# Optimization experiments

Measured on AMD Instinct MI355X. Metric: run time of the kernel, lower is better.

The kernel has to match this reference:

```python
import jax, jax.numpy as jnp
import numpy as np

B, S, D, H, L = 2, 4096, 768, 12, 4
DFF, WIN, MAXPOS = 3072, 256, 4098
DH = D // H
W1 = WIN // 2            # one-sided window = 128
NC = S // W1             # number of query chunks = 32
EPS = 1e-12              # LongformerConfig default layer_norm_eps
SCALE = 1.0 / float(np.sqrt(DH))


def _ln(x, g, b):
    m = x.mean(-1, keepdims=True)
    v = ((x - m) ** 2).mean(-1, keepdims=True)
    return (x - m) / jnp.sqrt(v + EPS) * g + b


def _fwd(inputs, lengths, pos_emb, tok_emb, ln_emb_g, ln_emb_b,
         Wq, bq, Wk, bk, Wv, bv, Wo, bo, ln1_g, ln1_b,
         Wi, bi, Wf, bf, ln2_g, ln2_b):
    # embeddings: roberta-style position ids start at padding_idx+1 = 2
    x = inputs + pos_emb[2:2 + S][None] + tok_emb[0][None, None]
    x = _ln(x, ln_emb_g, ln_emb_b)

    mask = jnp.arange(S)[None, :] < lengths[:, None]            # [B,S] valid tokens
    idx = jnp.arange(NC)[:, None] * W1 + jnp.arange(3 * W1)     # [NC,3W] into padded keys
    jglob = idx - W1                                            # global key positions
    key_valid = (jglob >= 0)[None] & (jglob[None] < lengths[:, None, None])  # [B,NC,3W]
    qpos = jnp.arange(W1)[:, None]
    kpos = jnp.arange(3 * W1)[None, :]
    band = (kpos >= qpos) & (kpos <= qpos + 2 * W1)             # [W,3W] sliding band
    valid = band[None, None, None] & key_valid[:, None, :, None, :]  # [B,1,NC,W,3W]
    qmask = mask.reshape(B, NC, W1).astype(inputs.dtype)

    for l in range(L):
        q = (x @ Wq[l] + bq[l]).reshape(B, S, H, DH) * SCALE
        k = (x @ Wk[l] + bk[l]).reshape(B, S, H, DH)
        v = (x @ Wv[l] + bv[l]).reshape(B, S, H, DH)
        kp = jnp.pad(k, ((0, 0), (W1, W1), (0, 0), (0, 0)))
        vp = jnp.pad(v, ((0, 0), (W1, W1), (0, 0), (0, 0)))
        kc = jnp.take(kp, idx, axis=1)                          # [B,NC,3W,H,DH]
        vc = jnp.take(vp, idx, axis=1)
        qc = q.reshape(B, NC, W1, H, DH)
        scores = jnp.einsum('bcqhd,bckhd->bhcqk', qc, kc)       # [B,H,NC,W,3W]
        scores = jnp.where(valid, scores, -1e9)
        probs = jax.nn.softmax(scores, axis=-1)
        probs = probs * qmask[:, None, :, :, None]              # zero padded query rows (HF behavior)
        ctx = jnp.einsum('bhcqk,bckhd->bcqhd', probs, vc).reshape(B, S, D)
        x = _ln(x + ctx @ Wo[l] + bo[l], ln1_g[l], ln1_b[l])
        h = jax.nn.gelu(x @ Wi[l] + bi[l], approximate=False)
        x = _ln(x + h @ Wf[l] + bf[l], ln2_g[l], ln2_b[l])
    return x


def setup_inputs() -> dict:
    ks = jax.random.split(jax.random.key(0), 16)
    s = jnp.float32(0.02)
    f = jax.random.normal
    return {
        'inputs': f(ks[0], (B, S, D), jnp.float32),
        'lengths': jax.random.randint(ks[1], (B,), S // 2, S + 1),
        'pos_emb': s * f(ks[2], (MAXPOS, D), jnp.float32),
        'tok_emb': s * f(ks[3], (1, D), jnp.float32),
        'ln_emb_g': jnp.ones((D,), jnp.float32), 'ln_emb_b': jnp.zeros((D,), jnp.float32),
        'Wq': s * f(ks[4], (L, D, D), jnp.float32), 'bq': jnp.zeros((L, D), jnp.float32),
        'Wk': s * f(ks[5], (L, D, D), jnp.float32), 'bk': jnp.zeros((L, D), jnp.float32),
        'Wv': s * f(ks[6], (L, D, D), jnp.float32), 'bv': jnp.zeros((L, D), jnp.float32),
        'Wo': s * f(ks[7], (L, D, D), jnp.float32), 'bo': jnp.zeros((L, D), jnp.float32),
        'ln1_g': jnp.ones((L, D), jnp.float32), 'ln1_b': jnp.zeros((L, D), jnp.float32),
        'Wi': s * f(ks[8], (L, D, DFF), jnp.float32), 'bi': jnp.zeros((L, DFF), jnp.float32),
        'Wf': s * f(ks[9], (L, DFF, D), jnp.float32), 'bf': jnp.zeros((L, D), jnp.float32),
        'ln2_g': jnp.ones((L, D), jnp.float32), 'ln2_b': jnp.zeros((L, D), jnp.float32),
    }


def reference(inputs, lengths, pos_emb, tok_emb, ln_emb_g, ln_emb_b,
              Wq, bq, Wk, bk, Wv, bv, Wo, bo, ln1_g, ln1_b,
              Wi, bi, Wf, bf, ln2_g, ln2_b):
    return _fwd(inputs, lengths, pos_emb, tok_emb, ln_emb_g, ln_emb_b,
                Wq, bq, Wk, bk, Wv, bv, Wo, bo, ln1_g, ln1_b,
                Wi, bi, Wf, bf, ln2_g, ln2_b)
```

## Files before the change

### kernel.cpp

```cpp
#include <hip/hip_runtime.h>
#include <cstdint>

#define S_LEN 4096
#define D_MODEL 768
#define NHEAD 12
#define DHE 64
#define DFF_ 3072
#define NL 4
#define W1_ 128
#define NC_ 32
#define QKVN 2304

typedef __attribute__((ext_vector_type(8))) short v8s;
typedef __attribute__((ext_vector_type(4))) short v4s;
typedef __attribute__((ext_vector_type(4))) float v4f;

__device__ __forceinline__ short f2bf(float f) {
  union { float f; unsigned u; } x; x.f = f;
  unsigned r = x.u + 0x7fffu + ((x.u >> 16) & 1u);
  return (short)(r >> 16);
}

__device__ __forceinline__ float b2f(short s) {
  union { unsigned u; float f; } x; x.u = ((unsigned)(unsigned short)s) << 16;
  return x.f;
}

__device__ __forceinline__ void load_lds16(const short* g, short* l) {
  __builtin_amdgcn_global_load_lds((const __attribute__((address_space(1))) void*)g,
                                   (__attribute__((address_space(3))) void*)l, 16, 0, 0);
}

template<int NB, int EPI, int WRV>
__global__ __launch_bounds__(512, 4)
void gemm128(const short* __restrict__ A, const short* __restrict__ Bt,
             const float* __restrict__ bias, void* __restrict__ outp,
             short* __restrict__ vtw, int M, int N, int K)
{
  constexpr int CF = NB / 64;
  constexpr int BI = NB / 64;
  constexpr int SI = 2 + BI;
  constexpr int ABUF = 128 * 64;
  constexpr int BBUF = NB * 64;
  __shared__ short sA[2 * ABUF];
  __shared__ short sB[2 * BBUF];
  const int tid = threadIdx.x;
  const int lane = tid & 63, wid = tid >> 6;
  const int g = lane >> 4, l16 = lane & 15;
  const int wr = wid >> 2, wc = wid & 3;
  const int nt = K >> 6;

  const int gx = gridDim.x;
  const int nwg = gx * gridDim.y;
  const int p = blockIdx.y * gx + blockIdx.x;
  const int q8 = nwg >> 3;
  const int lb = (p & 7) * q8 + (p >> 3);
  const int bn_ = lb % gx, bm_ = lb / gx;

  const short* Ab = A + (size_t)(bm_ * 128) * K;
  const short* Bb = Bt + (size_t)(bn_ * NB) * K;

  const short* gAp[2];
  short* lAp[2];
  const short* gBp[BI];
  short* lBp[BI];
#pragma unroll
  for (int i = 0; i < 2; ++i) {
    const int byte = i * 8192 + tid * 16;
    const int row = byte >> 7;
    const int lir = (byte & 127) ^ ((row & 7) << 4);
    gAp[i] = Ab + (size_t)row * K + (lir >> 1);
    lAp[i] = &sA[(i * 8192 + wid * 1024) >> 1];
  }
#pragma unroll
  for (int i = 0; i < BI; ++i) {
    const int byte = i * 8192 + tid * 16;
    const int row = byte >> 7;
    const int lir = (byte & 127) ^ ((row & 7) << 4);
    gBp[i] = Bb + (size_t)row * K + (lir >> 1);
    lBp[i] = &sB[(i * 8192 + wid * 1024) >> 1];
  }
  auto stage = [&](int bufi) {
#pragma unroll
    for (int i = 0; i < 2; ++i) {
      load_lds16(gAp[i], lAp[i] + bufi * ABUF);
      gAp[i] += 64;
    }
#pragma unroll
    for (int i = 0; i < BI; ++i) {
      load_lds16(gBp[i], lBp[i] + bufi * BBUF);
      gBp[i] += 64;
    }
  };

  const int swz = (l16 & 7) << 4;
  const char* aB[2];
  const char* bB[2];
#pragma unroll
  for (int kk = 0; kk < 2; ++kk) {
    const int koff = ((g * 16) ^ swz) ^ (kk * 64);
    aB[kk] = (const char*)sA + (wr * 64 + l16) * 128 + koff;
    bB[kk] = (const char*)sB + (wc * (CF * 16) + l16) * 128 + koff;
  }

  v4f acc[4][CF] = {};

  stage(0);
  stage(1);
  asm volatile("s_waitcnt vmcnt(%0)" :: "i"(SI) : "memory");
  __builtin_amdgcn_s_barrier();

#define GITER(CUR, T)                                                          \
  {                                                                            \
    v8s fa[2][4], fb[2][CF];                                                   \
    _Pragma("unroll")                                                          \
    for (int kk = 0; kk < 2; ++kk) {                                           \
      _Pragma("unroll")                                                        \
      for (int m = 0; m < 4; ++m)                                              \
        fa[kk][m] = *(const v8s*)(aB[kk] + (CUR) * (2 * ABUF) + m * 2048);     \
      _Pragma("unroll")                                                        \
      for (int n = 0; n < CF; ++n)                                             \
        fb[kk][n] = *(const v8s*)(bB[kk] + (CUR) * (2 * BBUF) + n * 2048);     \
    }                                                                          \
    asm volatile("s_waitcnt lgkmcnt(0)" ::: "memory");                         \
    __builtin_amdgcn_sched_barrier(0);                                         \
    __builtin_amdgcn_s_barrier();                                              \
    if ((T) + 2 < nt) stage(CUR);                                              \
    __builtin_amdgcn_sched_barrier(0);                                         \
    __builtin_amdgcn_s_setprio(1);                                             \
    _Pragma("unroll")                                                          \
    for (int kk = 0; kk < 2; ++kk)                                             \
      _Pragma("unroll")                                                        \
      for (int m = 0; m < 4; ++m)                                              \
        _Pragma("unroll")                                                      \
        for (int n = 0; n < CF; ++n)                                           \
          acc[m][n] = __builtin_amdgcn_mfma_f32_16x16x32_bf16(fa[kk][m], fb[kk][n], acc[m][n], 0, 0, 0); \
    __builtin_amdgcn_s_setprio(0);                                             \
    __builtin_amdgcn_sched_barrier(0);                                         \
    if ((T) + 2 < nt) {                                                        \
      asm volatile("s_waitcnt vmcnt(%0)" :: "i"(SI) : "memory");               \
    } else if ((T) + 1 < nt) {                                                 \
      asm volatile("s_waitcnt vmcnt(0)" ::: "memory");                         \
    }                                                                          \
    if ((T) + 1 < nt) __builtin_amdgcn_s_barrier();                            \
  }

  for (int t = 0; t < nt; t += 2) {
    GITER(0, t);
    GITER(1, t + 1);
  }
#undef GITER

  const int row0 = bm_ * 128 + wr * 64;
  const int col0 = bn_ * NB + wc * (CF * 16);
#pragma unroll
  for (int m = 0; m < 4; ++m)
#pragma unroll
    for (int n = 0; n < CF; ++n) {
      const int col = col0 + n * 16 + l16;
      const float bc = bias[col];
      short pk4[4];
#pragma unroll
      for (int r = 0; r < 4; ++r) {
        const int row = row0 + m * 16 + g * 4 + r;
        const float v = acc[m][n][r] + bc;
        short o;
        if (EPI == 2) {
          const float e = __expf(1.5957691216057308f * (v + 0.044715f * v * v * v));
          o = f2bf(v - v / (1.0f + e));
        } else {
          o = f2bf(v);
        }
        ((short*)outp)[(size_t)row * N + col] = o;
        pk4[r] = o;
      }
      if (WRV) {
        if (col0 >= 1536) {
          const int cc = col - 1536;
          const int h = cc >> 6, d = cc & 63;
          const int rowm = row0 + m * 16 + g * 4;
          const int b = rowm >> 12, s = rowm & (S_LEN - 1);
          v4s pk = { pk4[0], pk4[1], pk4[2], pk4[3] };
          *(v4s*)&vtw[(((size_t)b * NHEAD + h) * DHE + d) * S_LEN + s] = pk;
        }
      }
    }
}

__global__ __launch_bounds__(256)
void qkvo_trans(const float* __restrict__ Wq, const float* __restrict__ Wk,
                const float* __restrict__ Wv, const float* __restrict__ Wo,
                short* __restrict__ wqkvt, short* __restrict__ wot)
{
  __shared__ float t[32][33];
  const int n0 = blockIdx.x * 32, k0 = blockIdx.y * 32;
  const int l = blockIdx.z & 3, m = blockIdx.z >> 2;
  const size_t DD = (size_t)D_MODEL * D_MODEL;
  const size_t QL = (size_t)QKVN * D_MODEL;
  const float* src = (m == 0 ? Wq : m == 1 ? Wk : m == 2 ? Wv : Wo) + (size_t)l * DD;
  short* dst = (m < 3) ? (wqkvt + (size_t)l * QL + (size_t)m * D_MODEL * D_MODEL)
                       : (wot + (size_t)l * DD);
  const float scale = (m == 0) ? 0.125f : 1.0f;
  const int tx = threadIdx.x, ty = threadIdx.y;
#pragma unroll
  for (int i = 0; i < 4; ++i)
    t[ty + 8*i][tx] = src[(size_t)(k0 + ty + 8*i) * D_MODEL + n0 + tx];
  __syncthreads();
#pragma unroll
  for (int i = 0; i < 4; ++i)
    dst[(size_t)(n0 + ty + 8*i) * D_MODEL + k0 + tx] = f2bf(t[tx][ty + 8*i] * scale);
}

__global__ __launch_bounds__(256)
void transpose_w(const float* __restrict__ in, short* __restrict__ out, int K, int N,
                 size_t in_ls, size_t out_ls, float scale)
{
  __shared__ float t[32][33];
  const int n0 = blockIdx.x * 32, k0 = blockIdx.y * 32;
  const float* src = in + (size_t)blockIdx.z * in_ls;
  short* dst = out + (size_t)blockIdx.z * out_ls;
  const int tx = threadIdx.x, ty = threadIdx.y;
#pragma unroll
  for (int i = 0; i < 4; ++i)
    t[ty + 8*i][tx] = src[(size_t)(k0 + ty + 8*i) * N + n0 + tx];
  __syncthreads();
#pragma unroll
  for (int i = 0; i < 4; ++i)
    dst[(size_t)(n0 + ty + 8*i) * K + k0 + tx] = f2bf(t[tx][ty + 8*i] * scale);
}

__global__ void prep_bias(const float* __restrict__ bq, const float* __restrict__ bk,
                          const float* __restrict__ bv, float* __restrict__ out)
{
  const int l = blockIdx.x, p = blockIdx.y, c = threadIdx.x;
  const float* s = p == 0 ? bq : (p == 1 ? bk : bv);
  out[(l * 3 + p) * 768 + c] = s[l * 768 + c] * (p == 0 ? 0.125f : 1.0f);
}

template<int MODE, int FINAL>
__global__ __launch_bounds__(256)
void ln_kernel(const void* __restrict__ in0, const void* __restrict__ in1,
               const float* __restrict__ in2,
               const float* __restrict__ gamma, const float* __restrict__ beta,
               float* __restrict__ outf, short* __restrict__ outb)
{
  __shared__ float red[8];
  const int row = blockIdx.x;
  const int tid = threadIdx.x;
  const int wave = tid >> 6, lane = tid & 63;
  float v[3];
#pragma unroll
  for (int i = 0; i < 3; ++i) {
    const int c = tid + i * 256;
    const size_t idx = (size_t)row * D_MODEL + c;
    if (MODE == 0) {
      const int s = row & (S_LEN - 1);
      v[i] = ((const float*)in0)[idx] + ((const float*)in1)[(size_t)(2 + s) * D_MODEL + c] + in2[c];
    } else {
      v[i] = b2f(((const short*)in0)[idx]) + b2f(((const short*)in1)[idx]);
    }
  }
  float sum = v[0] + v[1] + v[2];
#pragma unroll
  for (int m = 1; m < 64; m <<= 1) sum += __shfl_xor(sum, m, 64);
  if (lane == 0) red[wave] = sum;
  __syncthreads();
  const float mean = (red[0] + red[1] + red[2] + red[3]) * (1.0f / 768.0f);
  float sq = 0.f;
#pragma unroll
  for (int i = 0; i < 3; ++i) { float d = v[i] - mean; sq += d * d; }
#pragma unroll
  for (int m = 1; m < 64; m <<= 1) sq += __shfl_xor(sq, m, 64);
  if (lane == 0) red[4 + wave] = sq;
  __syncthreads();
  const float var = (red[4] + red[5] + red[6] + red[7]) * (1.0f / 768.0f);
  const float rstd = 1.0f / sqrtf(var + 1e-12f);
#pragma unroll
  for (int i = 0; i < 3; ++i) {
    const int c = tid + i * 256;
    const size_t idx = (size_t)row * D_MODEL + c;
    const float o = (v[i] - mean) * rstd * gamma[c] + beta[c];
    if (FINAL) outf[idx] = o;
    outb[idx] = f2bf(o);
  }
}

__global__ __launch_bounds__(256, 2)
void att_fused(const short* __restrict__ qkv, const short* __restrict__ vt,
               const int* __restrict__ lengths, short* __restrict__ ctx)
{
  __shared__ __align__(16) short KP[320 * 64];
  __shared__ __align__(16) short Vl[64 * 320];
  const int p = blockIdx.x;
  const int lb = (p & 7) * 192 + (p >> 3);
  const int hq = lb & 1, c = (lb >> 1) & 31, bh = lb >> 6;
  const int b = bh / 12, h = bh - b * 12;
  const int len = lengths[b];
  const int tid = threadIdx.x;
  const int wave = tid >> 6, lane = tid & 63;
  const int g = lane >> 4, l16 = lane & 15;
  const int j0h = c * W1_ + hq * 64 - W1_;

  {
    const int row0 = tid >> 3;
    const int o = (tid & 7) * 16;
    const char* kcol = (const char*)qkv + (size_t)b * S_LEN * 4608 + 1536 + h * 128;
#pragma unroll
    for (int i = 0; i < 10; ++i) {
      const int r_ = i * 32 + row0;
      const int op = o ^ ((r_ & 7) << 4);
      int jg = j0h + r_;
      jg = jg < 0 ? 0 : (jg > S_LEN - 1 ? S_LEN - 1 : jg);
      load_lds16((const short*)(kcol + (size_t)jg * 4608 + op),
                 (short*)((char*)KP + i * 4096 + wave * 1024));
    }
  }
  __builtin_amdgcn_sched_barrier(0);
  const int qrow = c * W1_ + hq * 64 + wave * 16 + l16;
  const short* qp = qkv + (size_t)(b * S_LEN + qrow) * QKVN + h * DHE;
  const v8s a0 = *(const v8s*)(qp + g * 8);
  const v8s a1 = *(const v8s*)(qp + 32 + g * 8);
  __builtin_amdgcn_sched_barrier(0);
  {
    const char* vrow = (const char*)vt + ((size_t)(b * NHEAD + h) * DHE) * (S_LEN * 2);
#pragma unroll
    for (int r = 0; r < 10; ++r) {
      const int off = r * 4096 + tid * 16;
      const int rw = (int)(((unsigned)off * 6554u) >> 22);
      const int o = off - rw * 640;
      int jb = j0h * 2 + (o ^ ((rw & 7) << 4));
      jb = jb < 0 ? 0 : (jb > S_LEN * 2 - 16 ? S_LEN * 2 - 16 : jb);
      load_lds16((const short*)(vrow + (size_t)rw * (S_LEN * 2) + jb),
                 (short*)((char*)Vl + r * 4096 + wave * 1024));
    }
  }
  __builtin_amdgcn_sched_barrier(0);
  asm volatile("s_waitcnt vmcnt(10)" ::: "memory");
  __builtin_amdgcn_sched_barrier(0);
  __builtin_amdgcn_s_barrier();

  v4f s[20];
  const int kswz = (l16 & 7) << 4;
#pragma unroll
  for (int nt = 0; nt < 20; ++nt) {
    const char* krow = (const char*)KP + (nt * 16 + l16) * 128;
    const v8s k0 = *(const v8s*)(krow + ((g * 16) ^ kswz));
    const v8s k1 = *(const v8s*)(krow + ((64 + g * 16) ^ kswz));
    v4f t = {0.f, 0.f, 0.f, 0.f};
    t = __builtin_amdgcn_mfma_f32_16x16x32_bf16(k0, a0, t, 0, 0, 0);
    t = __builtin_amdgcn_mfma_f32_16x16x32_bf16(k1, a1, t, 0, 0, 0);
    s[nt] = t;
  }

  const int qloc = wave * 16 + l16;
  float m = -3.0e38f;
#pragma unroll
  for (int nt = 0; nt < 20; ++nt)
#pragma unroll
    for (int r = 0; r < 4; ++r) {
      const int j = nt * 16 + g * 4 + r;
      const int jg = j0h + j;
      const bool ok = (j >= qloc) & (j <= qloc + 2 * W1_) & (jg >= 0) & (jg < len);
      const float v = ok ? s[nt][r] : -1e9f;
      s[nt][r] = v;
      m = fmaxf(m, v);
    }
  m = fmaxf(m, __shfl_xor(m, 16, 64));
  m = fmaxf(m, __shfl_xor(m, 32, 64));
  float su = 0.f;
#pragma unroll
  for (int nt = 0; nt < 20; ++nt)
#pragma unroll
    for (int r = 0; r < 4; ++r) {
      const float e = __expf(s[nt][r] - m);
      s[nt][r] = e;
      su += e;
    }
  su += __shfl_xor(su, 16, 64);
  su += __shfl_xor(su, 32, 64);
  const float f = (qrow < len) ? 1.0f / su : 0.0f;

  asm volatile("s_waitcnt vmcnt(0)" ::: "memory");
  __builtin_amdgcn_sched_barrier(0);
  __builtin_amdgcn_s_barrier();
  const int pswz = (qloc & 7) << 4;
  char* prow = (char*)KP + qloc * 640;
#pragma unroll
  for (int nt = 0; nt < 20; ++nt) {
    v4s pk;
#pragma unroll
    for (int r = 0; r < 4; ++r) pk[r] = f2bf(s[nt][r] * f);
    *(v4s*)(prow + ((nt * 32 + g * 8) ^ pswz)) = pk;
  }
  asm volatile("s_waitcnt lgkmcnt(0)" ::: "memory");
  __builtin_amdgcn_sched_barrier(0);

  v4f acc[4] = {};
#pragma unroll
  for (int kc = 0; kc < 10; ++kc) {
    const v8s fa = *(const v8s*)(prow + ((kc * 64 + g * 16) ^ pswz));
#pragma unroll
    for (int dt = 0; dt < 4; ++dt) {
      const int vr = dt * 16 + l16;
      const v8s fb = *(const v8s*)((char*)Vl + vr * 640 + ((kc * 64 + g * 16) ^ ((vr & 7) << 4)));
      acc[dt] = __builtin_amdgcn_mfma_f32_16x16x32_bf16(fa, fb, acc[dt], 0, 0, 0);
    }
  }
  const int srow0 = c * W1_ + hq * 64 + wave * 16;
#pragma unroll
  for (int dt = 0; dt < 4; ++dt)
#pragma unroll
    for (int r = 0; r < 4; ++r)
      ctx[(size_t)(b * S_LEN + srow0 + g * 4 + r) * D_MODEL + h * DHE + dt * 16 + l16] = f2bf(acc[dt][r]);
}

extern "C" void kernel_launch(void* const* d_in, const int* in_sizes, int n_in,
                              void* d_out, int out_size, void* d_ws, size_t ws_size,
                              hipStream_t stream) {
  (void)in_sizes; (void)n_in; (void)out_size; (void)ws_size;
  const float* inputs  = (const float*)d_in[0];
  const int*   lengths = (const int*)d_in[1];
  const float* pos_emb = (const float*)d_in[2];
  const float* tok_emb = (const float*)d_in[3];
  const float* ln_emb_g = (const float*)d_in[4];
  const float* ln_emb_b = (const float*)d_in[5];
  const float* Wq = (const float*)d_in[6];
  const float* bq = (const float*)d_in[7];
  const float* Wk = (const float*)d_in[8];
  const float* bk = (const float*)d_in[9];
  const float* Wv = (const float*)d_in[10];
  const float* bv = (const float*)d_in[11];
  const float* Wo = (const float*)d_in[12];
  const float* bo = (const float*)d_in[13];
  const float* ln1_g = (const float*)d_in[14];
  const float* ln1_b = (const float*)d_in[15];
  const float* Wi = (const float*)d_in[16];
  const float* bi = (const float*)d_in[17];
  const float* Wf = (const float*)d_in[18];
  const float* bf2 = (const float*)d_in[19];
  const float* ln2_g = (const float*)d_in[20];
  const float* ln2_b = (const float*)d_in[21];

  const size_t MTOK = (size_t)2 * S_LEN;
  const size_t DD  = (size_t)D_MODEL * D_MODEL;
  const size_t DDF = (size_t)D_MODEL * DFF_;

  char* ws = (char*)d_ws;
  size_t off = 0;
  auto alloc = [&](size_t bytes) { void* p = ws + off; off += (bytes + 255) & ~(size_t)255; return p; };

  short* xb    = (short*)alloc(MTOK * D_MODEL * 2);
  short* qkv   = (short*)alloc(MTOK * QKVN * 2);
  short* vtb   = (short*)alloc(MTOK * D_MODEL * 2);
  short* yb    = (short*)alloc(MTOK * D_MODEL * 2);
  short* ctxb  = (short*)alloc(MTOK * D_MODEL * 2);
  short* hb    = (short*)alloc(MTOK * DFF_ * 2);
  short* wqkvt = (short*)alloc((size_t)NL * QKVN * D_MODEL * 2);
  short* wot   = (short*)alloc((size_t)NL * DD * 2);
  short* wit   = (short*)alloc((size_t)NL * DDF * 2);
  short* wft   = (short*)alloc((size_t)NL * DDF * 2);
  float* bqkv  = (float*)alloc((size_t)NL * QKVN * 4);
  float* x = (float*)d_out;

  const dim3 tb(32, 8);
  const size_t QL = (size_t)QKVN * D_MODEL;
  qkvo_trans<<<dim3(24, 24, 16), tb, 0, stream>>>(Wq, Wk, Wv, Wo, wqkvt, wot);
  transpose_w<<<dim3(96, 24, NL), tb, 0, stream>>>(Wi, wit, D_MODEL, DFF_, DDF, DDF, 1.0f);
  transpose_w<<<dim3(24, 96, NL), tb, 0, stream>>>(Wf, wft, DFF_, D_MODEL, DDF, DDF, 1.0f);
  prep_bias<<<dim3(NL, 3), 768, 0, stream>>>(bq, bk, bv, bqkv);

  ln_kernel<0, 0><<<MTOK, 256, 0, stream>>>(inputs, pos_emb, tok_emb, ln_emb_g, ln_emb_b, x, xb);

  for (int l = 0; l < NL; ++l) {
    gemm128<128, 0, 1><<<dim3(18, 64), 512, 0, stream>>>(xb, wqkvt + (size_t)l * QL, bqkv + (size_t)l * QKVN,
                                                         qkv, vtb, (int)MTOK, QKVN, D_MODEL);
    att_fused<<<dim3(1536), 256, 0, stream>>>(qkv, vtb, lengths, ctxb);
    gemm128<64, 0, 0><<<dim3(12, 64), 512, 0, stream>>>(ctxb, wot + (size_t)l * DD, bo + l * D_MODEL,
                                                        yb, nullptr, (int)MTOK, D_MODEL, D_MODEL);
    ln_kernel<1, 0><<<MTOK, 256, 0, stream>>>(xb, yb, nullptr, ln1_g + l * D_MODEL, ln1_b + l * D_MODEL, x, xb);
    gemm128<128, 2, 0><<<dim3(24, 64), 512, 0, stream>>>(xb, wit + (size_t)l * DDF, bi + l * DFF_,
                                                         hb, nullptr, (int)MTOK, DFF_, D_MODEL);
    gemm128<64, 0, 0><<<dim3(12, 64), 512, 0, stream>>>(hb, wft + (size_t)l * DDF, bf2 + l * D_MODEL,
                                                        yb, nullptr, (int)MTOK, D_MODEL, DFF_);
    if (l < NL - 1)
      ln_kernel<1, 0><<<MTOK, 256, 0, stream>>>(xb, yb, nullptr, ln2_g + l * D_MODEL, ln2_b + l * D_MODEL, x, xb);
    else
      ln_kernel<1, 1><<<MTOK, 256, 0, stream>>>(xb, yb, nullptr, ln2_g + l * D_MODEL, ln2_b + l * D_MODEL, x, xb);
  }
}
```

Before: 848.5 us.

## Convert GEMM kernels to persistent grid with tile loop

The GEMM kernel becomes persistent: a fixed 1-D grid of workgroups (512 or 768) loops over logical output tiles, with the logical grid width and tile count passed as arguments. The QKV and FFN-up GEMMs now run in multiple waves inside each block instead of as separate block launches, while the 768-tile GEMMs keep a one-to-one mapping. The aim is to cut launch and tail imbalance costs and keep the XCD-aware tile mapping. The risk is lost overlap between tiles, since each new tile restarts its prologue without prefetching the next one, and the chosen grid size may underfill the device.

```diff
diff --git a/kernel.cpp b/kernel.cpp
--- a/kernel.cpp
+++ b/kernel.cpp
@@ -35,7 +35,7 @@
 __global__ __launch_bounds__(512, 4)
 void gemm128(const short* __restrict__ A, const short* __restrict__ Bt,
              const float* __restrict__ bias, void* __restrict__ outp,
-             short* __restrict__ vtw, int M, int N, int K)
+             short* __restrict__ vtw, int M, int N, int K, int gxl, int nwgl)
 {
   constexpr int CF = NB / 64;
   constexpr int BI = NB / 64;
@@ -50,26 +50,20 @@
   const int wr = wid >> 2, wc = wid & 3;
   const int nt = K >> 6;
 
-  const int gx = gridDim.x;
-  const int nwg = gx * gridDim.y;
-  const int p = blockIdx.y * gx + blockIdx.x;
-  const int q8 = nwg >> 3;
-  const int lb = (p & 7) * q8 + (p >> 3);
-  const int bn_ = lb % gx, bm_ = lb / gx;
-
-  const short* Ab = A + (size_t)(bm_ * 128) * K;
-  const short* Bb = Bt + (size_t)(bn_ * NB) * K;
-
-  const short* gAp[2];
+  const int PHYS = gridDim.x;
+  const int q8 = PHYS >> 3;
+  const int slot = (blockIdx.x & 7) * q8 + (blockIdx.x >> 3);
+
+  int aoffE[2];
   short* lAp[2];
-  const short* gBp[BI];
+  int boffE[BI];
   short* lBp[BI];
 #pragma unroll
   for (int i = 0; i < 2; ++i) {
     const int byte = i * 8192 + tid * 16;
     const int row = byte >> 7;
     const int lir = (byte & 127) ^ ((row & 7) << 4);
-    gAp[i] = Ab + (size_t)row * K + (lir >> 1);
+    aoffE[i] = row * K + (lir >> 1);
     lAp[i] = &sA[(i * 8192 + wid * 1024) >> 1];
   }
 #pragma unroll
@@ -77,21 +71,9 @@
     const int byte = i * 8192 + tid * 16;
     const int row = byte >> 7;
     const int lir = (byte & 127) ^ ((row & 7) << 4);
-    gBp[i] = Bb + (size_t)row * K + (lir >> 1);
+    boffE[i] = row * K + (lir >> 1);
     lBp[i] = &sB[(i * 8192 + wid * 1024) >> 1];
   }
-  auto stage = [&](int bufi) {
-#pragma unroll
-    for (int i = 0; i < 2; ++i) {
-      load_lds16(gAp[i], lAp[i] + bufi * ABUF);
-      gAp[i] += 64;
-    }
-#pragma unroll
-    for (int i = 0; i < BI; ++i) {
-      load_lds16(gBp[i], lBp[i] + bufi * BBUF);
-      gBp[i] += 64;
-    }
-  };
 
   const int swz = (l16 & 7) << 4;
   const char* aB[2];
@@ -103,12 +85,38 @@
     bB[kk] = (const char*)sB + (wc * (CF * 16) + l16) * 128 + koff;
   }
 
-  v4f acc[4][CF] = {};
-
-  stage(0);
-  stage(1);
-  asm volatile("s_waitcnt vmcnt(%0)" :: "i"(SI) : "memory");
-  __builtin_amdgcn_s_barrier();
+  for (int base = 0; base + slot < nwgl; base += PHYS) {
+    const int lb = base + slot;
+    const int bn_ = lb % gxl, bm_ = lb / gxl;
+    const short* Ab = A + (size_t)(bm_ * 128) * K;
+    const short* Bb = Bt + (size_t)(bn_ * NB) * K;
+
+    const short* gAp[2];
+    const short* gBp[BI];
+#pragma unroll
+    for (int i = 0; i < 2; ++i) gAp[i] = Ab + aoffE[i];
+#pragma unroll
+    for (int i = 0; i < BI; ++i) gBp[i] = Bb + boffE[i];
+
+    auto stage = [&](int bufi) {
+#pragma unroll
+      for (int i = 0; i < 2; ++i) {
+        load_lds16(gAp[i], lAp[i] + bufi * ABUF);
+        gAp[i] += 64;
+      }
+#pragma unroll
+      for (int i = 0; i < BI; ++i) {
+        load_lds16(gBp[i], lBp[i] + bufi * BBUF);
+        gBp[i] += 64;
+      }
+    };
+
+    v4f acc[4][CF] = {};
+
+    stage(0);
+    stage(1);
+    asm volatile("s_waitcnt vmcnt(%0)" :: "i"(SI) : "memory");
+    __builtin_amdgcn_s_barrier();
 
 #define GITER(CUR, T)                                                          \
   {                                                                            \
@@ -145,46 +153,47 @@
     if ((T) + 1 < nt) __builtin_amdgcn_s_barrier();                            \
   }
 
-  for (int t = 0; t < nt; t += 2) {
-    GITER(0, t);
-    GITER(1, t + 1);
-  }
+    for (int t = 0; t < nt; t += 2) {
+      GITER(0, t);
+      GITER(1, t + 1);
+    }
 #undef GITER
 
-  const int row0 = bm_ * 128 + wr * 64;
-  const int col0 = bn_ * NB + wc * (CF * 16);
-#pragma unroll
-  for (int m = 0; m < 4; ++m)
-#pragma unroll
-    for (int n = 0; n < CF; ++n) {
-      const int col = col0 + n * 16 + l16;
-      const float bc = bias[col];
-      short pk4[4];
-#pragma unroll
-      for (int r = 0; r < 4; ++r) {
-        const int row = row0 + m * 16 + g * 4 + r;
-        const float v = acc[m][n][r] + bc;
-        short o;
-        if (EPI == 2) {
-          const float e = __expf(1.5957691216057308f * (v + 0.044715f * v * v * v));
-          o = f2bf(v - v / (1.0f + e));
-        } else {
-          o = f2bf(v);
+    const int row0 = bm_ * 128 + wr * 64;
+    const int col0 = bn_ * NB + wc * (CF * 16);
+#pragma unroll
+    for (int m = 0; m < 4; ++m)
+#pragma unroll
+      for (int n = 0; n < CF; ++n) {
+        const int col = col0 + n * 16 + l16;
+        const float bc = bias[col];
+        short pk4[4];
+#pragma unroll
+        for (int r = 0; r < 4; ++r) {
+          const int row = row0 + m * 16 + g * 4 + r;
+          const float v = acc[m][n][r] + bc;
+          short o;
+          if (EPI == 2) {
+            const float e = __expf(1.5957691216057308f * (v + 0.044715f * v * v * v));
+            o = f2bf(v - v / (1.0f + e));
+          } else {
+            o = f2bf(v);
+          }
+          ((short*)outp)[(size_t)row * N + col] = o;
+          pk4[r] = o;
         }
-        ((short*)outp)[(size_t)row * N + col] = o;
-        pk4[r] = o;
-      }
-      if (WRV) {
-        if (col0 >= 1536) {
-          const int cc = col - 1536;
-          const int h = cc >> 6, d = cc & 63;
-          const int rowm = row0 + m * 16 + g * 4;
-          const int b = rowm >> 12, s = rowm & (S_LEN - 1);
-          v4s pk = { pk4[0], pk4[1], pk4[2], pk4[3] };
-          *(v4s*)&vtw[(((size_t)b * NHEAD + h) * DHE + d) * S_LEN + s] = pk;
+        if (WRV) {
+          if (col0 >= 1536) {
+            const int cc = col - 1536;
+            const int h = cc >> 6, d = cc & 63;
+            const int rowm = row0 + m * 16 + g * 4;
+            const int b = rowm >> 12, s = rowm & (S_LEN - 1);
+            v4s pk = { pk4[0], pk4[1], pk4[2], pk4[3] };
+            *(v4s*)&vtw[(((size_t)b * NHEAD + h) * DHE + d) * S_LEN + s] = pk;
+          }
         }
       }
-    }
+  }
 }
 
 __global__ __launch_bounds__(256)
@@ -472,16 +481,16 @@
   ln_kernel<0, 0><<<MTOK, 256, 0, stream>>>(inputs, pos_emb, tok_emb, ln_emb_g, ln_emb_b, x, xb);
 
   for (int l = 0; l < NL; ++l) {
-    gemm128<128, 0, 1><<<dim3(18, 64), 512, 0, stream>>>(xb, wqkvt + (size_t)l * QL, bqkv + (size_t)l * QKVN,
-                                                         qkv, vtb, (int)MTOK, QKVN, D_MODEL);
+    gemm128<128, 0, 1><<<dim3(512), 512, 0, stream>>>(xb, wqkvt + (size_t)l * QL, bqkv + (size_t)l * QKVN,
+                                                      qkv, vtb, (int)MTOK, QKVN, D_MODEL, 18, 1152);
     att_fused<<<dim3(1536), 256, 0, stream>>>(qkv, vtb, lengths, ctxb);
-    gemm128<64, 0, 0><<<dim3(12, 64), 512, 0, stream>>>(ctxb, wot + (size_t)l * DD, bo + l * D_MODEL,
-                                                        yb, nullptr, (int)MTOK, D_MODEL, D_MODEL);
+    gemm128<64, 0, 0><<<dim3(768), 512, 0, stream>>>(ctxb, wot + (size_t)l * DD, bo + l * D_MODEL,
+                                                     yb, nullptr, (int)MTOK, D_MODEL, D_MODEL, 12, 768);
     ln_kernel<1, 0><<<MTOK, 256, 0, stream>>>(xb, yb, nullptr, ln1_g + l * D_MODEL, ln1_b + l * D_MODEL, x, xb);
-    gemm128<128, 2, 0><<<dim3(24, 64), 512, 0, stream>>>(xb, wit + (size_t)l * DDF, bi + l * DFF_,
-                                                         hb, nullptr, (int)MTOK, DFF_, D_MODEL);
-    gemm128<64, 0, 0><<<dim3(12, 64), 512, 0, stream>>>(hb, wft + (size_t)l * DDF, bf2 + l * D_MODEL,
-                                                        yb, nullptr, (int)MTOK, D_MODEL, DFF_);
+    gemm128<128, 2, 0><<<dim3(512), 512, 0, stream>>>(xb, wit + (size_t)l * DDF, bi + l * DFF_,
+                                                      hb, nullptr, (int)MTOK, DFF_, D_MODEL, 24, 1536);
+    gemm128<64, 0, 0><<<dim3(768), 512, 0, stream>>>(hb, wft + (size_t)l * DDF, bf2 + l * D_MODEL,
+                                                     yb, nullptr, (int)MTOK, D_MODEL, DFF_, 12, 768);
     if (l < NL - 1)
       ln_kernel<1, 0><<<MTOK, 256, 0, stream>>>(xb, yb, nullptr, ln2_g + l * D_MODEL, ln2_b + l * D_MODEL, x, xb);
     else
```

Result: slower. 887.1 us (+4.6%).
